# Optimization experiments

Measured on AMD Instinct MI355X. Metric: run time of the kernel, lower is better.

## Reference

```python
import jax, jax.numpy as jnp
import numpy as np

H_DIM, W_DIM, D_MODEL = 128, 128, 1024
N_HEADS, HEAD_DIM = 16, 64


def setup_inputs() -> dict:
    key = jax.random.key(0)
    ks = jax.random.split(key, 8)
    s = D_MODEL ** -0.5
    return {
        "hidden_state": jax.random.normal(ks[0], (H_DIM, W_DIM, D_MODEL), jnp.float32),
        "attn_mask": jnp.zeros((1, 1, W_DIM, W_DIM), jnp.float32),
        "cos": jax.random.uniform(ks[1], (H_DIM, W_DIM, 1, HEAD_DIM), jnp.float32),
        "sin": jax.random.uniform(ks[2], (H_DIM, W_DIM, 1, HEAD_DIM), jnp.float32),
        "Wq": jax.random.normal(ks[3], (D_MODEL, N_HEADS * HEAD_DIM), jnp.float32) * s,
        "Wk": jax.random.normal(ks[4], (D_MODEL, N_HEADS * HEAD_DIM), jnp.float32) * s,
        "Wv": jax.random.normal(ks[5], (D_MODEL, N_HEADS * HEAD_DIM), jnp.float32) * s,
        "Wo": jax.random.normal(ks[6], (2 * D_MODEL, D_MODEL), jnp.float32) * s,
    }


def _rotate_half(x):
    x1, x2 = jnp.split(x, 2, axis=-1)
    return jnp.concatenate((-x2, x1), axis=-1)


def reference(hidden_state, attn_mask, cos, sin, Wq, Wk, Wv, Wo):
    h, w, d = hidden_state.shape
    Dh = cos.shape[-1]
    nH = d // Dh
    # projections (no bias) + RoPE on q/k
    q = (hidden_state @ Wq).reshape(h, w, nH, Dh)
    k = (hidden_state @ Wk).reshape(h, w, nH, Dh)
    v = (hidden_state @ Wv).reshape(h, w, nH, Dh)
    q = q * cos + _rotate_half(q) * sin
    k = k * cos + _rotate_half(k) * sin
    # NOTE: original divides by sqrt(hidden_size), not sqrt(head_dim)
    scale = jnp.sqrt(jnp.asarray(d, hidden_state.dtype))
    # ---- width attention: (h, w, nH, Dh) -> (h, nH, w, Dh) ----
    qx, kx, vx = (t.transpose(0, 2, 1, 3) for t in (q, k, v))
    sx = jnp.einsum('ahqd,ahkd->ahqk', qx, kx) / scale + attn_mask  # (h, nH, w, w)
    ow = jnp.einsum('ahqk,ahkd->ahqd', jax.nn.softmax(sx, axis=-1), vx)
    w_weights = ow.transpose(0, 2, 1, 3)  # (h, w, nH, Dh)
    # ---- height attention: (h, w, nH, Dh) -> (w, nH, h, Dh) ----
    qy, ky, vy = (t.transpose(1, 2, 0, 3) for t in (q, k, v))
    my = jnp.transpose(attn_mask, (2, 1, 0, 3))
    sy = jnp.einsum('ahqd,ahkd->ahqk', qy, ky) / scale + my  # (w, nH, h, h)
    oh = jnp.einsum('ahqk,ahkd->ahqd', jax.nn.softmax(sy, axis=-1), vy)
    h_weights = oh.transpose(2, 0, 1, 3)  # (h, w, nH, Dh)
    cat = jnp.concatenate([w_weights.reshape(h, w, d), h_weights.reshape(h, w, d)], axis=-1)
    return cat @ Wo
```

## Files before the change

### kernel.cpp

```cpp
#include <hip/hip_runtime.h>

typedef unsigned short u16;
typedef unsigned int   u32;
typedef __bf16 bf16;
typedef bf16  bf16x8 __attribute__((ext_vector_type(8)));
typedef float f32x4  __attribute__((ext_vector_type(4)));

__device__ __forceinline__ u16 bf16u(float f) {
    u32 x = __builtin_bit_cast(u32, f);
    x += 0x7fffu + ((x >> 16) & 1u);
    return (u16)(x >> 16);
}

__device__ __forceinline__ void gl_lds16(const void* g, void* l) {
    __builtin_amdgcn_global_load_lds(
        (const __attribute__((address_space(1))) u32*)g,
        (__attribute__((address_space(3))) u32*)l, 16, 0, 0);
}

__global__ __launch_bounds__(256) void cvt_x_kernel(const float4* __restrict__ in,
                                                    ushort4* __restrict__ out, int n4) {
    int i = blockIdx.x * 256 + threadIdx.x;
    if (i >= n4) return;
    float4 f = in[i];
    ushort4 o;
    o.x = bf16u(f.x); o.y = bf16u(f.y); o.z = bf16u(f.z); o.w = bf16u(f.w);
    out[i] = o;
}

__global__ __launch_bounds__(256) void transp_all(
    const float* __restrict__ Wq, const float* __restrict__ Wk,
    const float* __restrict__ Wv, const float* __restrict__ Wo,
    u16* __restrict__ WqkvT, u16* __restrict__ WoT)
{
    const int z = blockIdx.z;
    const float* W; u16* WT; int rows, cols;
    if (z < 3) {
        if (blockIdx.y >= 32) return;
        W = (z == 0) ? Wq : (z == 1) ? Wk : Wv;
        WT = WqkvT + (size_t)z * 1024 * 1024;
        rows = 1024; cols = 1024;
    } else {
        W = Wo; WT = WoT; rows = 2048; cols = 1024;
    }
    __shared__ float t[32][33];
    int bx = blockIdx.x * 32, by = blockIdx.y * 32;
    int x = threadIdx.x & 31, y = threadIdx.x >> 5;
#pragma unroll
    for (int i = 0; i < 32; i += 8)
        t[y + i][x] = W[(size_t)(by + y + i) * cols + bx + x];
    __syncthreads();
#pragma unroll
    for (int i = 0; i < 32; i += 8)
        WT[(size_t)(bx + y + i) * rows + by + x] = bf16u(t[x][y + i]);
}

__global__ __launch_bounds__(256) void gemm97(
    const u16* __restrict__ A, const u16* __restrict__ BT, void* __restrict__ Cout,
    const float* __restrict__ cosp, const float* __restrict__ sinp,
    int M, int N, int K, int mode)
{
    __shared__ u16 Ld[8192];
    const int tid = threadIdx.x;
    const int wid = tid >> 6, lane = tid & 63;
    const int nx = gridDim.x;
    const int nwg = nx * gridDim.y;
    const int orig = blockIdx.y * nx + blockIdx.x;
    const int vid = (orig & 7) * (nwg >> 3) + (orig >> 3);
    const int m0 = (vid / nx) << 7, n0 = (vid % nx) << 7;
    const int wr = wid >> 1, wc = wid & 1;

    const int srow = tid >> 2;
    const int sg = (tid & 3) ^ ((srow >> 1) & 3);
    const u16* aS = A + (size_t)(m0 + srow) * K + (sg << 3);
    const u16* bS = BT + (size_t)(n0 + srow) * K + (sg << 3);
    const size_t h64K = (size_t)64 * K;
    const int wdb = wid << 9;
    const int nt = K >> 5;

    const int phys = ((lane >> 4) ^ ((lane >> 1) & 3)) << 3;
    const int raw = ((wr << 6) + (lane & 15)) << 5;
    const int rbw = (((wc << 6) + (lane & 15)) << 5) + 4096;

    f32x4 acc[4][4] = {};

    for (int t = 0; t < nt; ++t) {
        if (t) __syncthreads();
        const size_t ko = (size_t)t << 5;
        gl_lds16(aS + ko,        &Ld[wdb]);
        gl_lds16(aS + ko + h64K, &Ld[2048 + wdb]);
        gl_lds16(bS + ko,        &Ld[4096 + wdb]);
        gl_lds16(bS + ko + h64K, &Ld[6144 + wdb]);
        __syncthreads();

        bf16x8 af[4], bfr[4];
#pragma unroll
        for (int i = 0; i < 4; i++)
            af[i] = *(const bf16x8*)&Ld[raw + (i << 9) + phys];
#pragma unroll
        for (int i = 0; i < 4; i++)
            bfr[i] = *(const bf16x8*)&Ld[rbw + (i << 9) + phys];
        __builtin_amdgcn_s_setprio(1);
#pragma unroll
        for (int mi = 0; mi < 4; mi++)
#pragma unroll
            for (int ni = 0; ni < 4; ni++)
                acc[mi][ni] = __builtin_amdgcn_mfma_f32_16x16x32_bf16(
                    af[mi], bfr[ni], acc[mi][ni], 0, 0, 0);
        __builtin_amdgcn_s_setprio(0);
    }

    const int colbase = n0 + (wc << 6) + (lane & 15);
    if (mode == 2) {
        float* C = (float*)Cout;
#pragma unroll
        for (int mi = 0; mi < 4; mi++)
#pragma unroll
            for (int r = 0; r < 4; r++) {
                int m = m0 + (wr << 6) + (mi << 4) + ((lane >> 4) << 2) + r;
                float* row = C + (size_t)m * N + colbase;
#pragma unroll
                for (int ni = 0; ni < 4; ni++) row[ni << 4] = acc[mi][ni][r];
            }
    } else if (n0 < 2048) {
        u16* C = (u16*)Cout;
#pragma unroll
        for (int mi = 0; mi < 4; mi++)
#pragma unroll
            for (int r = 0; r < 4; r++) {
                int m = m0 + (wr << 6) + (mi << 4) + ((lane >> 4) << 2) + r;
                const float* cb = cosp + ((size_t)m << 6);
                const float* sb = sinp + ((size_t)m << 6);
                u16* row = C + (size_t)m * N + colbase;
#pragma unroll
                for (int ni = 0; ni < 4; ni++) {
                    int d = (ni << 4) + (lane & 15);
                    float c = cb[d], s = sb[d];
                    float v0 = acc[mi][ni][r];
                    float vr = acc[mi][ni ^ 2][r];
                    float o = fmaf(v0, c, (ni < 2 ? -vr : vr) * s);
                    row[ni << 4] = bf16u(o);
                }
            }
    } else {
        u16* C = (u16*)Cout;
#pragma unroll
        for (int mi = 0; mi < 4; mi++)
#pragma unroll
            for (int r = 0; r < 4; r++) {
                int m = m0 + (wr << 6) + (mi << 4) + ((lane >> 4) << 2) + r;
                u16* row = C + (size_t)m * N + colbase;
#pragma unroll
                for (int ni = 0; ni < 4; ni++) row[ni << 4] = bf16u(acc[mi][ni][r]);
            }
    }
}

__global__ __launch_bounds__(256) void axial_attn(
    const u16* __restrict__ qkv, const float* __restrict__ mask,
    u16* __restrict__ cat)
{
    __shared__ u16 Kl[128 * 64];
    __shared__ u16 VT[64 * 128];
    __shared__ u16 Pl[128 * 128];
    const int hmode = blockIdx.x >> 11;
    const int o2 = blockIdx.x & 2047;
    const int b = (o2 & 7) * 256 + (o2 >> 3);
    const int a = b >> 4, hd = b & 15;
    const int tid = threadIdx.x, wid = tid >> 6, lane = tid & 63;
    const int tmul = hmode ? 128 : 1;
    const int tadd = hmode ? a : (a << 7);
    const size_t hoff = (size_t)hd << 6;

#pragma unroll
    for (int c = 0; c < 4; c++) {
        int row = (wid << 5) + (c << 3) + (lane >> 3);
        int sc = (lane & 7) ^ (row & 7);
        gl_lds16(qkv + (size_t)(row * tmul + tadd) * 3072 + 1024 + hoff + (sc << 3),
                 &Kl[((wid << 5) + (c << 3)) << 6]);
    }
#pragma unroll
    for (int i = 0; i < 4; i++) {
        int cid = tid + (i << 8);
        int j = cid >> 3;
        int d0 = (cid & 7) << 3;
        uint4 raw = *(const uint4*)(qkv + (size_t)(j * tmul + tadd) * 3072 + 2048 + hoff + d0);
        const u16* e = (const u16*)&raw;
#pragma unroll
        for (int t = 0; t < 8; t++) {
            int d = d0 + t;
            VT[(d << 7) + (((j >> 3) ^ (d & 15)) << 3) + (j & 7)] = e[t];
        }
    }
    bf16x8 aq[2][2];
#pragma unroll
    for (int qt = 0; qt < 2; qt++)
#pragma unroll
        for (int ks = 0; ks < 2; ks++) {
            int row = (wid << 5) + (qt << 4) + (lane & 15);
            aq[qt][ks] = *(const bf16x8*)(qkv + (size_t)(row * tmul + tadd) * 3072 + hoff
                                          + (ks << 5) + ((lane >> 4) << 3));
        }
    __syncthreads();

    f32x4 S[2][8] = {};
#pragma unroll
    for (int kt = 0; kt < 8; kt++) {
        bf16x8 bk[2];
#pragma unroll
        for (int ks = 0; ks < 2; ks++) {
            int row = (kt << 4) + (lane & 15);
            int ch = ((ks << 2) + (lane >> 4)) ^ (row & 7);
            bk[ks] = *(const bf16x8*)&Kl[(row << 6) + (ch << 3)];
        }
#pragma unroll
        for (int qt = 0; qt < 2; qt++) {
            S[qt][kt] = __builtin_amdgcn_mfma_f32_16x16x32_bf16(aq[qt][0], bk[0], S[qt][kt], 0, 0, 0);
            S[qt][kt] = __builtin_amdgcn_mfma_f32_16x16x32_bf16(aq[qt][1], bk[1], S[qt][kt], 0, 0, 0);
        }
    }

    const float scale = 0.03125f;
#pragma unroll
    for (int qt = 0; qt < 2; qt++) {
#pragma unroll
        for (int r = 0; r < 4; r++) {
            int qrow = (wid << 5) + (qt << 4) + ((lane >> 4) << 2) + r;
            const float* mrow = mask + (hmode ? (a << 7) : (qrow << 7));
            float mx = -1e30f;
#pragma unroll
            for (int kt = 0; kt < 8; kt++) {
                float sv = fmaf(S[qt][kt][r], scale, mrow[(kt << 4) + (lane & 15)]);
                S[qt][kt][r] = sv;
                mx = fmaxf(mx, sv);
            }
            mx = fmaxf(mx, __shfl_xor(mx, 1));
            mx = fmaxf(mx, __shfl_xor(mx, 2));
            mx = fmaxf(mx, __shfl_xor(mx, 4));
            mx = fmaxf(mx, __shfl_xor(mx, 8));
            float sum = 0.f;
#pragma unroll
            for (int kt = 0; kt < 8; kt++) {
                float p = __expf(S[qt][kt][r] - mx);
                S[qt][kt][r] = p;
                sum += p;
            }
            sum += __shfl_xor(sum, 1);
            sum += __shfl_xor(sum, 2);
            sum += __shfl_xor(sum, 4);
            sum += __shfl_xor(sum, 8);
            float rinv = 1.0f / sum;
#pragma unroll
            for (int kt = 0; kt < 8; kt++) {
                int kcol = (kt << 4) + (lane & 15);
                int ch = (kcol >> 3) ^ (qrow & 15);
                Pl[(qrow << 7) + (ch << 3) + (kcol & 7)] = bf16u(S[qt][kt][r] * rinv);
            }
        }
    }
    __syncthreads();

    f32x4 O[4][2] = {};
#pragma unroll
    for (int ks = 0; ks < 4; ks++) {
        bf16x8 av[4], bp[2];
#pragma unroll
        for (int dt = 0; dt < 4; dt++) {
            int drow = (dt << 4) + (lane & 15);
            int ch = ((ks << 2) + (lane >> 4)) ^ (drow & 15);
            av[dt] = *(const bf16x8*)&VT[(drow << 7) + (ch << 3)];
        }
#pragma unroll
        for (int qt = 0; qt < 2; qt++) {
            int qrow = (wid << 5) + (qt << 4) + (lane & 15);
            int ch = ((ks << 2) + (lane >> 4)) ^ (qrow & 15);
            bp[qt] = *(const bf16x8*)&Pl[(qrow << 7) + (ch << 3)];
        }
#pragma unroll
        for (int dt = 0; dt < 4; dt++)
#pragma unroll
            for (int qt = 0; qt < 2; qt++)
                O[dt][qt] = __builtin_amdgcn_mfma_f32_16x16x32_bf16(av[dt], bp[qt], O[dt][qt], 0, 0, 0);
    }

    const int cbase = (hmode ? 1024 : 0) + (hd << 6);
#pragma unroll
    for (int dt = 0; dt < 4; dt++)
#pragma unroll
        for (int qt = 0; qt < 2; qt++) {
            int qrow = (wid << 5) + (qt << 4) + (lane & 15);
            int d0 = (dt << 4) + ((lane >> 4) << 2);
            size_t base = ((size_t)(qrow * tmul + tadd) << 11) + cbase + d0;
            ushort4 pk;
            pk.x = bf16u(O[dt][qt][0]);
            pk.y = bf16u(O[dt][qt][1]);
            pk.z = bf16u(O[dt][qt][2]);
            pk.w = bf16u(O[dt][qt][3]);
            *(ushort4*)(cat + base) = pk;
        }
}

extern "C" void kernel_launch(void* const* d_in, const int* in_sizes, int n_in,
                              void* d_out, int out_size, void* d_ws, size_t ws_size,
                              hipStream_t stream)
{
    (void)in_sizes; (void)n_in; (void)out_size; (void)ws_size;
    const float* hidden = (const float*)d_in[0];
    const float* mask   = (const float*)d_in[1];
    const float* cosp   = (const float*)d_in[2];
    const float* sinp   = (const float*)d_in[3];
    const float* Wq     = (const float*)d_in[4];
    const float* Wk     = (const float*)d_in[5];
    const float* Wv     = (const float*)d_in[6];
    const float* Wo     = (const float*)d_in[7];

    char* ws = (char*)d_ws;
    u16* Xb    = (u16*)(ws);
    u16* WqkvT = (u16*)(ws + 33554432);
    u16* cat   = (u16*)(ws);
    u16* WoT   = (u16*)(ws + 67108864);
    u16* qkvb  = (u16*)(ws + 71303168);

    cvt_x_kernel<<<16384, 256, 0, stream>>>((const float4*)hidden, (ushort4*)Xb, 4194304);
    transp_all<<<dim3(32, 64, 4), 256, 0, stream>>>(Wq, Wk, Wv, Wo, WqkvT, WoT);

    gemm97<<<dim3(24, 128), 256, 0, stream>>>(Xb, WqkvT, qkvb, cosp, sinp, 16384, 3072, 1024, 1);

    axial_attn<<<4096, 256, 0, stream>>>(qkvb, mask, cat);

    gemm97<<<dim3(8, 128), 256, 0, stream>>>(cat, WoT, d_out, nullptr, nullptr, 16384, 1024, 2048, 2);
}
```

Before: 348.6 us.

## Load GEMM B operand directly to registers with double-buffered prefetch

The GEMM kernel now stages only the A tile through LDS. Each wave loads its B fragments straight from global memory into registers, prefetching the next K-step's B while computing the current one (two register buffers, loop unrolled by 2). Shared memory is halved and launch bounds request 3 blocks per CU to raise occupancy. The cost is that B is read redundantly by the two waves sharing a column block, through uncoalesced 16-byte loads rather than LDS-staged ones, plus extra registers and barriers.

```diff
diff --git a/kernel.cpp b/kernel.cpp
--- a/kernel.cpp
+++ b/kernel.cpp
@@ -55,12 +55,12 @@
         WT[(size_t)(bx + y + i) * rows + by + x] = bf16u(t[x][y + i]);
 }
 
-__global__ __launch_bounds__(256) void gemm97(
+__global__ __launch_bounds__(256, 3) void gemm_bd(
     const u16* __restrict__ A, const u16* __restrict__ BT, void* __restrict__ Cout,
     const float* __restrict__ cosp, const float* __restrict__ sinp,
     int M, int N, int K, int mode)
 {
-    __shared__ u16 Ld[8192];
+    __shared__ u16 Ld[4096];
     const int tid = threadIdx.x;
     const int wid = tid >> 6, lane = tid & 63;
     const int nx = gridDim.x;
@@ -73,42 +73,58 @@
     const int srow = tid >> 2;
     const int sg = (tid & 3) ^ ((srow >> 1) & 3);
     const u16* aS = A + (size_t)(m0 + srow) * K + (sg << 3);
-    const u16* bS = BT + (size_t)(n0 + srow) * K + (sg << 3);
     const size_t h64K = (size_t)64 * K;
     const int wdb = wid << 9;
     const int nt = K >> 5;
 
+    const u16* Bb = BT + (size_t)(n0 + (wc << 6) + (lane & 15)) * K
+                       + ((lane >> 4) << 3);
+    const size_t bstep = (size_t)16 * K;
+
     const int phys = ((lane >> 4) ^ ((lane >> 1) & 3)) << 3;
     const int raw = ((wr << 6) + (lane & 15)) << 5;
-    const int rbw = (((wc << 6) + (lane & 15)) << 5) + 4096;
 
     f32x4 acc[4][4] = {};
-
-    for (int t = 0; t < nt; ++t) {
+    bf16x8 b0[4], b1[4];
+
+#define STAGEA(T) do { const size_t _ko = (size_t)(T) << 5; \
+        gl_lds16(aS + _ko,        &Ld[wdb]); \
+        gl_lds16(aS + _ko + h64K, &Ld[2048 + wdb]); } while (0)
+#define LOADB(DST, T) do { const size_t _ko = (size_t)(T) << 5; \
+        DST[0] = *(const bf16x8*)(Bb + _ko); \
+        DST[1] = *(const bf16x8*)(Bb + bstep + _ko); \
+        DST[2] = *(const bf16x8*)(Bb + 2 * bstep + _ko); \
+        DST[3] = *(const bf16x8*)(Bb + 3 * bstep + _ko); } while (0)
+#define COMPUTE(BREG) do { \
+        bf16x8 af[4]; \
+        _Pragma("unroll") \
+        for (int i = 0; i < 4; i++) \
+            af[i] = *(const bf16x8*)&Ld[raw + (i << 9) + phys]; \
+        __builtin_amdgcn_s_setprio(1); \
+        _Pragma("unroll") \
+        for (int mi = 0; mi < 4; mi++) \
+            _Pragma("unroll") \
+            for (int ni = 0; ni < 4; ni++) \
+                acc[mi][ni] = __builtin_amdgcn_mfma_f32_16x16x32_bf16( \
+                    af[mi], BREG[ni], acc[mi][ni], 0, 0, 0); \
+        __builtin_amdgcn_s_setprio(0); } while (0)
+
+    LOADB(b0, 0);
+    for (int t = 0; t < nt; t += 2) {
         if (t) __syncthreads();
-        const size_t ko = (size_t)t << 5;
-        gl_lds16(aS + ko,        &Ld[wdb]);
-        gl_lds16(aS + ko + h64K, &Ld[2048 + wdb]);
-        gl_lds16(bS + ko,        &Ld[4096 + wdb]);
-        gl_lds16(bS + ko + h64K, &Ld[6144 + wdb]);
+        STAGEA(t);
+        if (t + 1 < nt) LOADB(b1, t + 1);
         __syncthreads();
-
-        bf16x8 af[4], bfr[4];
-#pragma unroll
-        for (int i = 0; i < 4; i++)
-            af[i] = *(const bf16x8*)&Ld[raw + (i << 9) + phys];
-#pragma unroll
-        for (int i = 0; i < 4; i++)
-            bfr[i] = *(const bf16x8*)&Ld[rbw + (i << 9) + phys];
-        __builtin_amdgcn_s_setprio(1);
-#pragma unroll
-        for (int mi = 0; mi < 4; mi++)
-#pragma unroll
-            for (int ni = 0; ni < 4; ni++)
-                acc[mi][ni] = __builtin_amdgcn_mfma_f32_16x16x32_bf16(
-                    af[mi], bfr[ni], acc[mi][ni], 0, 0, 0);
-        __builtin_amdgcn_s_setprio(0);
-    }
+        COMPUTE(b0);
+        __syncthreads();
+        STAGEA(t + 1);
+        if (t + 2 < nt) LOADB(b0, t + 2);
+        __syncthreads();
+        COMPUTE(b1);
+    }
+#undef STAGEA
+#undef LOADB
+#undef COMPUTE
 
     const int colbase = n0 + (wc << 6) + (lane & 15);
     if (mode == 2) {
@@ -324,9 +340,9 @@
     cvt_x_kernel<<<16384, 256, 0, stream>>>((const float4*)hidden, (ushort4*)Xb, 4194304);
     transp_all<<<dim3(32, 64, 4), 256, 0, stream>>>(Wq, Wk, Wv, Wo, WqkvT, WoT);
 
-    gemm97<<<dim3(24, 128), 256, 0, stream>>>(Xb, WqkvT, qkvb, cosp, sinp, 16384, 3072, 1024, 1);
+    gemm_bd<<<dim3(24, 128), 256, 0, stream>>>(Xb, WqkvT, qkvb, cosp, sinp, 16384, 3072, 1024, 1);
 
     axial_attn<<<4096, 256, 0, stream>>>(qkvb, mask, cat);
 
-    gemm97<<<dim3(8, 128), 256, 0, stream>>>(cat, WoT, d_out, nullptr, nullptr, 16384, 1024, 2048, 2);
-}
+    gemm_bd<<<dim3(8, 128), 256, 0, stream>>>(cat, WoT, d_out, nullptr, nullptr, 16384, 1024, 2048, 2);
+}
```

Result: slower. 496.6 us (+42.5%).

## Multi-buffer GEMM LDS with prefetch of next two K-tiles

Applied to the files above, without the earlier changes.

Replaces the single-buffer GEMM main loop with a 4-slot LDS ring. The loads for the next two K-tiles are issued before computing the current two, with one barrier per pair of tiles. This is meant to overlap global-to-LDS loads with MFMA work and halve barrier count. It quadruples LDS use per block to 64KB and adds launch_bounds occupancy hint 2. Occupancy may drop.

```diff
diff --git a/kernel.cpp b/kernel.cpp
--- a/kernel.cpp
+++ b/kernel.cpp
@@ -55,12 +55,15 @@
         WT[(size_t)(bx + y + i) * rows + by + x] = bf16u(t[x][y + i]);
 }
 
-__global__ __launch_bounds__(256) void gemm97(
+#define BAR   __builtin_amdgcn_s_barrier()
+#define VM0   asm volatile("s_waitcnt vmcnt(0)" ::: "memory")
+
+__global__ __launch_bounds__(256, 2) void gemm_pp(
     const u16* __restrict__ A, const u16* __restrict__ BT, void* __restrict__ Cout,
     const float* __restrict__ cosp, const float* __restrict__ sinp,
     int M, int N, int K, int mode)
 {
-    __shared__ u16 Ld[8192];
+    __shared__ u16 Ld[4][8192];
     const int tid = threadIdx.x;
     const int wid = tid >> 6, lane = tid & 63;
     const int nx = gridDim.x;
@@ -78,37 +81,63 @@
     const int wdb = wid << 9;
     const int nt = K >> 5;
 
+#define STAGE(T) do { const int _b = (T) & 3; const size_t _ko = (size_t)(T) << 5; \
+        gl_lds16(aS + _ko,        &Ld[_b][wdb]); \
+        gl_lds16(aS + _ko + h64K, &Ld[_b][2048 + wdb]); \
+        gl_lds16(bS + _ko,        &Ld[_b][4096 + wdb]); \
+        gl_lds16(bS + _ko + h64K, &Ld[_b][6144 + wdb]); } while (0)
+
     const int phys = ((lane >> 4) ^ ((lane >> 1) & 3)) << 3;
     const int raw = ((wr << 6) + (lane & 15)) << 5;
     const int rbw = (((wc << 6) + (lane & 15)) << 5) + 4096;
 
     f32x4 acc[4][4] = {};
 
-    for (int t = 0; t < nt; ++t) {
-        if (t) __syncthreads();
-        const size_t ko = (size_t)t << 5;
-        gl_lds16(aS + ko,        &Ld[wdb]);
-        gl_lds16(aS + ko + h64K, &Ld[2048 + wdb]);
-        gl_lds16(bS + ko,        &Ld[4096 + wdb]);
-        gl_lds16(bS + ko + h64K, &Ld[6144 + wdb]);
-        __syncthreads();
-
-        bf16x8 af[4], bfr[4];
-#pragma unroll
-        for (int i = 0; i < 4; i++)
-            af[i] = *(const bf16x8*)&Ld[raw + (i << 9) + phys];
-#pragma unroll
-        for (int i = 0; i < 4; i++)
-            bfr[i] = *(const bf16x8*)&Ld[rbw + (i << 9) + phys];
-        __builtin_amdgcn_s_setprio(1);
-#pragma unroll
-        for (int mi = 0; mi < 4; mi++)
-#pragma unroll
-            for (int ni = 0; ni < 4; ni++)
-                acc[mi][ni] = __builtin_amdgcn_mfma_f32_16x16x32_bf16(
-                    af[mi], bfr[ni], acc[mi][ni], 0, 0, 0);
-        __builtin_amdgcn_s_setprio(0);
-    }
+    STAGE(0); STAGE(1);
+    VM0; BAR;
+
+    for (int t = 0; t < nt; t += 2) {
+        if (t + 2 < nt) STAGE(t + 2);
+        if (t + 3 < nt) STAGE(t + 3);
+        {
+            const u16* Lb = &Ld[t & 3][0];
+            bf16x8 af[4], bfr[4];
+#pragma unroll
+            for (int i = 0; i < 4; i++)
+                af[i] = *(const bf16x8*)&Lb[raw + (i << 9) + phys];
+#pragma unroll
+            for (int i = 0; i < 4; i++)
+                bfr[i] = *(const bf16x8*)&Lb[rbw + (i << 9) + phys];
+            __builtin_amdgcn_s_setprio(1);
+#pragma unroll
+            for (int mi = 0; mi < 4; mi++)
+#pragma unroll
+                for (int ni = 0; ni < 4; ni++)
+                    acc[mi][ni] = __builtin_amdgcn_mfma_f32_16x16x32_bf16(
+                        af[mi], bfr[ni], acc[mi][ni], 0, 0, 0);
+            __builtin_amdgcn_s_setprio(0);
+        }
+        {
+            const u16* Lb = &Ld[(t + 1) & 3][0];
+            bf16x8 af[4], bfr[4];
+#pragma unroll
+            for (int i = 0; i < 4; i++)
+                af[i] = *(const bf16x8*)&Lb[raw + (i << 9) + phys];
+#pragma unroll
+            for (int i = 0; i < 4; i++)
+                bfr[i] = *(const bf16x8*)&Lb[rbw + (i << 9) + phys];
+            __builtin_amdgcn_s_setprio(1);
+#pragma unroll
+            for (int mi = 0; mi < 4; mi++)
+#pragma unroll
+                for (int ni = 0; ni < 4; ni++)
+                    acc[mi][ni] = __builtin_amdgcn_mfma_f32_16x16x32_bf16(
+                        af[mi], bfr[ni], acc[mi][ni], 0, 0, 0);
+            __builtin_amdgcn_s_setprio(0);
+        }
+        VM0; BAR;
+    }
+#undef STAGE
 
     const int colbase = n0 + (wc << 6) + (lane & 15);
     if (mode == 2) {
@@ -324,9 +353,9 @@
     cvt_x_kernel<<<16384, 256, 0, stream>>>((const float4*)hidden, (ushort4*)Xb, 4194304);
     transp_all<<<dim3(32, 64, 4), 256, 0, stream>>>(Wq, Wk, Wv, Wo, WqkvT, WoT);
 
-    gemm97<<<dim3(24, 128), 256, 0, stream>>>(Xb, WqkvT, qkvb, cosp, sinp, 16384, 3072, 1024, 1);
+    gemm_pp<<<dim3(24, 128), 256, 0, stream>>>(Xb, WqkvT, qkvb, cosp, sinp, 16384, 3072, 1024, 1);
 
     axial_attn<<<4096, 256, 0, stream>>>(qkvb, mask, cat);
 
-    gemm97<<<dim3(8, 128), 256, 0, stream>>>(cat, WoT, d_out, nullptr, nullptr, 16384, 1024, 2048, 2);
-}
+    gemm_pp<<<dim3(8, 128), 256, 0, stream>>>(cat, WoT, d_out, nullptr, nullptr, 16384, 1024, 2048, 2);
+}
```

Result: faster. 331.1 us (-5.0%).

## Double GEMM K-tile to 64 with new LDS swizzle and merge prep kernels

Applied to the files above, without the earlier changes.

The GEMM now stages a 64-wide K slice per iteration (32 KB LDS) instead of 32. It uses a new XOR swizzle and runs two MFMA sub-steps per barrier, which halves the number of sync/load rounds. The hidden-state bf16 conversion is folded into the weight-transpose kernel as an extra z-slice, saving one launch. In exchange, the doubled LDS use may lower occupancy and the new swizzle could add bank conflicts.

```diff
diff --git a/kernel.cpp b/kernel.cpp
--- a/kernel.cpp
+++ b/kernel.cpp
@@ -18,22 +18,26 @@
         (__attribute__((address_space(3))) u32*)l, 16, 0, 0);
 }
 
-__global__ __launch_bounds__(256) void cvt_x_kernel(const float4* __restrict__ in,
-                                                    ushort4* __restrict__ out, int n4) {
-    int i = blockIdx.x * 256 + threadIdx.x;
-    if (i >= n4) return;
-    float4 f = in[i];
-    ushort4 o;
-    o.x = bf16u(f.x); o.y = bf16u(f.y); o.z = bf16u(f.z); o.w = bf16u(f.w);
-    out[i] = o;
-}
-
-__global__ __launch_bounds__(256) void transp_all(
+__global__ __launch_bounds__(256) void prep_all(
+    const float* __restrict__ hidden, ushort4* __restrict__ Xb,
     const float* __restrict__ Wq, const float* __restrict__ Wk,
     const float* __restrict__ Wv, const float* __restrict__ Wo,
     u16* __restrict__ WqkvT, u16* __restrict__ WoT)
 {
     const int z = blockIdx.z;
+    if (z == 4) {
+        const float4* in = (const float4*)hidden;
+        int b = blockIdx.y * 32 + blockIdx.x;
+#pragma unroll
+        for (int it = 0; it < 8; it++) {
+            int i = (b << 11) + (it << 8) + threadIdx.x;
+            float4 f = in[i];
+            ushort4 o;
+            o.x = bf16u(f.x); o.y = bf16u(f.y); o.z = bf16u(f.z); o.w = bf16u(f.w);
+            Xb[i] = o;
+        }
+        return;
+    }
     const float* W; u16* WT; int rows, cols;
     if (z < 3) {
         if (blockIdx.y >= 32) return;
@@ -55,12 +59,12 @@
         WT[(size_t)(bx + y + i) * rows + by + x] = bf16u(t[x][y + i]);
 }
 
-__global__ __launch_bounds__(256) void gemm97(
+__global__ __launch_bounds__(256) void gemm_sb(
     const u16* __restrict__ A, const u16* __restrict__ BT, void* __restrict__ Cout,
     const float* __restrict__ cosp, const float* __restrict__ sinp,
     int M, int N, int K, int mode)
 {
-    __shared__ u16 Ld[8192];
+    __shared__ u16 Ld[16384];
     const int tid = threadIdx.x;
     const int wid = tid >> 6, lane = tid & 63;
     const int nx = gridDim.x;
@@ -70,36 +74,58 @@
     const int m0 = (vid / nx) << 7, n0 = (vid % nx) << 7;
     const int wr = wid >> 1, wc = wid & 1;
 
-    const int srow = tid >> 2;
-    const int sg = (tid & 3) ^ ((srow >> 1) & 3);
-    const u16* aS = A + (size_t)(m0 + srow) * K + (sg << 3);
-    const u16* bS = BT + (size_t)(n0 + srow) * K + (sg << 3);
-    const size_t h64K = (size_t)64 * K;
-    const int wdb = wid << 9;
-    const int nt = K >> 5;
-
-    const int phys = ((lane >> 4) ^ ((lane >> 1) & 3)) << 3;
-    const int raw = ((wr << 6) + (lane & 15)) << 5;
-    const int rbw = (((wc << 6) + (lane & 15)) << 5) + 4096;
+    const int crow0 = (wid << 5) + (lane >> 3);
+    const int sg0 = (lane & 7);
+    const size_t rK[4] = {
+        (size_t)(crow0) * K,       (size_t)(crow0 + 8) * K,
+        (size_t)(crow0 + 16) * K,  (size_t)(crow0 + 24) * K };
+    int gsl[4];
+#pragma unroll
+    for (int i = 0; i < 4; i++) gsl[i] = (sg0 ^ ((crow0 + 8 * i) & 7)) << 3;
+    const u16* aB = A + (size_t)m0 * K;
+    const u16* bB = BT + (size_t)n0 * K;
+    const int dstA = (wid << 11);
+    const int nt = K >> 6;
+
+    const int ph0 = (((lane >> 4))     ^ (lane & 7)) << 3;
+    const int ph1 = (((lane >> 4) + 4) ^ (lane & 7)) << 3;
+    const int raw = ((wr << 6) + (lane & 15)) << 6;
+    const int rbw = (((wc << 6) + (lane & 15)) << 6) + 8192;
 
     f32x4 acc[4][4] = {};
 
     for (int t = 0; t < nt; ++t) {
         if (t) __syncthreads();
-        const size_t ko = (size_t)t << 5;
-        gl_lds16(aS + ko,        &Ld[wdb]);
-        gl_lds16(aS + ko + h64K, &Ld[2048 + wdb]);
-        gl_lds16(bS + ko,        &Ld[4096 + wdb]);
-        gl_lds16(bS + ko + h64K, &Ld[6144 + wdb]);
+        const size_t ko = (size_t)t << 6;
+#pragma unroll
+        for (int i = 0; i < 4; i++)
+            gl_lds16(aB + rK[i] + ko + gsl[i], &Ld[dstA + (i << 9)]);
+#pragma unroll
+        for (int i = 0; i < 4; i++)
+            gl_lds16(bB + rK[i] + ko + gsl[i], &Ld[8192 + dstA + (i << 9)]);
         __syncthreads();
 
         bf16x8 af[4], bfr[4];
 #pragma unroll
         for (int i = 0; i < 4; i++)
-            af[i] = *(const bf16x8*)&Ld[raw + (i << 9) + phys];
-#pragma unroll
-        for (int i = 0; i < 4; i++)
-            bfr[i] = *(const bf16x8*)&Ld[rbw + (i << 9) + phys];
+            af[i] = *(const bf16x8*)&Ld[raw + (i << 10) + ph0];
+#pragma unroll
+        for (int i = 0; i < 4; i++)
+            bfr[i] = *(const bf16x8*)&Ld[rbw + (i << 10) + ph0];
+        __builtin_amdgcn_s_setprio(1);
+#pragma unroll
+        for (int mi = 0; mi < 4; mi++)
+#pragma unroll
+            for (int ni = 0; ni < 4; ni++)
+                acc[mi][ni] = __builtin_amdgcn_mfma_f32_16x16x32_bf16(
+                    af[mi], bfr[ni], acc[mi][ni], 0, 0, 0);
+        __builtin_amdgcn_s_setprio(0);
+#pragma unroll
+        for (int i = 0; i < 4; i++)
+            af[i] = *(const bf16x8*)&Ld[raw + (i << 10) + ph1];
+#pragma unroll
+        for (int i = 0; i < 4; i++)
+            bfr[i] = *(const bf16x8*)&Ld[rbw + (i << 10) + ph1];
         __builtin_amdgcn_s_setprio(1);
 #pragma unroll
         for (int mi = 0; mi < 4; mi++)
@@ -321,12 +347,12 @@
     u16* WoT   = (u16*)(ws + 67108864);
     u16* qkvb  = (u16*)(ws + 71303168);
 
-    cvt_x_kernel<<<16384, 256, 0, stream>>>((const float4*)hidden, (ushort4*)Xb, 4194304);
-    transp_all<<<dim3(32, 64, 4), 256, 0, stream>>>(Wq, Wk, Wv, Wo, WqkvT, WoT);
-
-    gemm97<<<dim3(24, 128), 256, 0, stream>>>(Xb, WqkvT, qkvb, cosp, sinp, 16384, 3072, 1024, 1);
+    prep_all<<<dim3(32, 64, 5), 256, 0, stream>>>(hidden, (ushort4*)Xb,
+                                                  Wq, Wk, Wv, Wo, WqkvT, WoT);
+
+    gemm_sb<<<dim3(24, 128), 256, 0, stream>>>(Xb, WqkvT, qkvb, cosp, sinp, 16384, 3072, 1024, 1);
 
     axial_attn<<<4096, 256, 0, stream>>>(qkvb, mask, cat);
 
-    gemm97<<<dim3(8, 128), 256, 0, stream>>>(cat, WoT, d_out, nullptr, nullptr, 16384, 1024, 2048, 2);
-}
+    gemm_sb<<<dim3(8, 128), 256, 0, stream>>>(cat, WoT, d_out, nullptr, nullptr, 16384, 1024, 2048, 2);
+}
```

After: 325.3 us. 1.07x faster.
